# Performance work log

Measured on AMD Instinct MI355X. Metric: run time of the kernel, lower is better.

The kernel has to match this reference:

```python
import jax, jax.numpy as jnp
import numpy as np
import math

B, S, D, H, WD = 8, 2048, 512, 8, 64
DK = D // H


def setup_inputs() -> dict:
    k = jax.random.key(0)
    ks = jax.random.split(k, 16)
    s = 0.02
    return {
        "query": jax.random.normal(ks[0], (B, S, D), jnp.float32),
        "key": jax.random.normal(ks[1], (B, S, D), jnp.float32),
        "value": jax.random.normal(ks[2], (B, S, D), jnp.float32),
        "mask": jax.random.randint(ks[3], (B, S), 0, 2, jnp.int32),
        "segment_weights": jax.random.uniform(ks[4], (B, S, S), jnp.float32),
        # torch Linear weights: [out_features, in_features]
        "Wq": jax.random.normal(ks[5], (D, D), jnp.float32) * s,
        "bq": jnp.zeros((D,), jnp.float32),
        "Wk": jax.random.normal(ks[6], (D, D), jnp.float32) * s,
        "bk": jnp.zeros((D,), jnp.float32),
        "Wv": jax.random.normal(ks[7], (D, D), jnp.float32) * s,
        "bv": jnp.zeros((D,), jnp.float32),
        "Wo": jax.random.normal(ks[8], (D, D), jnp.float32) * s,
        "bo": jnp.zeros((D,), jnp.float32),
        "Wl": jax.random.normal(ks[9], (WD, 1), jnp.float32) * 0.1,
        "bl": jnp.zeros((WD,), jnp.float32),
        "Wr": jax.random.normal(ks[10], (1, WD), jnp.float32) * 0.1,
        "br": jnp.zeros((1,), jnp.float32),
    }


def reference(query, key, value, mask, segment_weights,
              Wq, bq, Wk, bk, Wv, bv, Wo, bo, Wl, bl, Wr, br):
    nb = query.shape[0]
    # segment bias MLP: 1 -> WD -> 1 with leaky_relu(0.2)
    sw = 1.0 / jnp.log(jnp.float32(math.e) + segment_weights)  # [B,S,S]
    hmid = jax.nn.leaky_relu(sw[..., None] * Wl[:, 0] + bl, negative_slope=0.2)  # [B,S,S,WD]
    bias = (hmid @ Wr.T + br)[..., 0]  # [B,S,S]

    def proj(x, W, b):
        return (x @ W.T + b).reshape(nb, -1, H, DK).transpose(0, 2, 1, 3)  # [B,H,S,DK]

    q = proj(query, Wq, bq)
    k = proj(key, Wk, bk)
    v = proj(value, Wv, bv)

    scores = jnp.einsum("bhqd,bhkd->bhqk", q, k) / jnp.float32(math.sqrt(DK))
    scores = scores + bias[:, None]  # broadcast over heads
    # mask [B,S] -> [B,1,S,1]: masks query rows (as in original)
    scores = jnp.where(mask[:, None, :, None] == 0, jnp.float32(-1e9), scores)
    p = jax.nn.softmax(scores, axis=-1)
    x = jnp.einsum("bhqk,bhkd->bhqd", p, v)
    x = x.transpose(0, 2, 1, 3).reshape(nb, -1, H * DK)
    return x @ Wo.T + bo
```

## Files before the change

### kernel.cpp

```cpp
#include <hip/hip_runtime.h>
#include <stdint.h>

#define Bb 8
#define Ss 2048
#define Dd 512
#define Hh 8

typedef unsigned short u16;
typedef __attribute__((ext_vector_type(8))) short s16x8;
typedef __attribute__((ext_vector_type(4))) unsigned short u16x4;
typedef __attribute__((ext_vector_type(4))) float f32x4;
typedef __attribute__((ext_vector_type(2))) float f32x2;

__device__ __forceinline__ u16 f2bf(float f){
  unsigned u = __float_as_uint(f);
  return (u16)((u + 0x7fffu + ((u>>16)&1u)) >> 16);
}

__device__ __forceinline__ unsigned cvtpk_bf16(float lo, float hi){
  unsigned r;
  asm("v_cvt_pk_bf16_f32 %0, %1, %2" : "=v"(r) : "v"(lo), "v"(hi));
  return r;
}

__device__ __forceinline__ void gl_lds16(const void* g, void* l){
  __builtin_amdgcn_global_load_lds((const __attribute__((address_space(1))) unsigned int*)g,
                                   (__attribute__((address_space(3))) unsigned int*)l, 16, 0, 0);
}

#define MFMA32(a,b,c) __builtin_amdgcn_mfma_f32_16x16x32_bf16(a,b,c,0,0,0)

__global__ __launch_bounds__(256) void castw(const float* __restrict__ a, const float* __restrict__ b,
                                             const float* __restrict__ c, const float* __restrict__ d,
                                             u16* __restrict__ o){
  int i = blockIdx.x*256 + threadIdx.x;
  const float* src = (i < 65536) ? a : (i < 131072) ? b : (i < 196608) ? c : d;
  int off = (i & 65535) << 2;
  f32x4 v = *(const f32x4*)(src + off);
  u16x4 r;
  #pragma unroll
  for(int j = 0; j < 4; j++) r[j] = f2bf(v[j]);
  *(u16x4*)(o + ((size_t)(i >> 16) << 18) + off) = r;
}

__global__ void prep(const float* __restrict__ Wl, const float* __restrict__ bl,
                     const float* __restrict__ Wr, const float* __restrict__ br,
                     float* __restrict__ consts){
  int w = threadIdx.x;
  float wl = Wl[w], blv = bl[w], wr = Wr[w];
  float h0 = 0.75f*wl + blv; h0 = h0 > 0.f ? h0 : 0.2f*h0;
  float h1 = 1.00f*wl + blv; h1 = h1 > 0.f ? h1 : 0.2f*h1;
  float f0 = wr*h0, f1 = wr*h1;
  #pragma unroll
  for(int off = 32; off > 0; off >>= 1){
    f0 += __shfl_down(f0, off);
    f1 += __shfl_down(f1, off);
  }
  if(w == 0){
    const float L2E = 1.4426950408889634f;
    float brv = br[0];
    float F0 = f0 + brv, F1 = f1 + brv;
    float C1 = (F1 - F0) * 4.0f;
    float C0 = F0 - 0.75f*C1;
    consts[0] = C1 * L2E * L2E;
    consts[1] = C0 * L2E;
  }
}

template<int MODE>
__global__ __launch_bounds__(256) void gemm_t(const void* __restrict__ Ap, const u16* __restrict__ W,
                                              const float* __restrict__ bias, void* __restrict__ Cp){
  __shared__ __align__(16) u16 As[128*32];
  __shared__ __align__(16) u16 Bs[128*32];
  const int t = threadIdx.x;
  const int lane = t & 63, wv = t >> 6;
  const int quad = lane >> 4, l15 = lane & 15;
  const int m0 = blockIdx.x * 128, n0 = blockIdx.y * 128;
  const int R = (wv >> 1) * 64, Cc = (wv & 1) * 64;
  f32x4 acc[4][4] = {};
  for(int kb = 0; kb < 512; kb += 32){
    __syncthreads();
    #pragma unroll
    for(int i = 0; i < 2; i++){
      int u  = i*256 + t;
      int m  = u >> 2;
      int cc = (u & 3) ^ ((m >> 1) & 3);
      if (MODE == 2){
        gl_lds16((const u16*)Ap + (size_t)(m0 + m)*512 + kb + cc*8, As + (size_t)(i*256 + wv*64)*8);
      } else {
        const float* src = (const float*)Ap + (size_t)(m0 + m)*512 + kb + cc*8;
        f32x4 v0 = *(const f32x4*)src;
        f32x4 v1 = *(const f32x4*)(src + 4);
        s16x8 cv;
        #pragma unroll
        for(int r2 = 0; r2 < 4; r2++){ cv[r2] = (short)f2bf(v0[r2]); cv[4+r2] = (short)f2bf(v1[r2]); }
        *(s16x8*)(As + (size_t)u*8) = cv;
      }
      gl_lds16(W + (size_t)(n0 + m)*512 + kb + cc*8, Bs + (size_t)(i*256 + wv*64)*8);
    }
    __syncthreads();
    s16x8 af[4], bfr[4];
    #pragma unroll
    for(int mi = 0; mi < 4; mi++){
      int m = R + mi*16 + l15;
      int u = (m << 2) | (quad ^ ((m >> 1) & 3));
      af[mi] = *(const s16x8*)(As + (size_t)u*8);
    }
    #pragma unroll
    for(int ni = 0; ni < 4; ni++){
      int n = Cc + ni*16 + l15;
      int u = (n << 2) | (quad ^ ((n >> 1) & 3));
      bfr[ni] = *(const s16x8*)(Bs + (size_t)u*8);
    }
    #pragma unroll
    for(int mi = 0; mi < 4; mi++)
      #pragma unroll
      for(int ni = 0; ni < 4; ni++)
        acc[mi][ni] = MFMA32(af[mi], bfr[ni], acc[mi][ni]);
  }
  #pragma unroll
  for(int ni = 0; ni < 4; ni++){
    int col = n0 + Cc + ni*16 + l15;
    float bv = bias[col];
    #pragma unroll
    for(int mi = 0; mi < 4; mi++){
      int row0 = m0 + R + mi*16 + quad*4;
      #pragma unroll
      for(int r = 0; r < 4; r++){
        float v = acc[mi][ni][r] + bv;
        int row = row0 + r;
        if (MODE == 2)      ((float*)Cp)[(size_t)row*512 + col] = v;
        else if (MODE == 1) ((u16*)Cp)[(size_t)((row >> 11)*512 + col)*2048 + (size_t)(row & 2047)] = f2bf(v);
        else                ((u16*)Cp)[(size_t)row*512 + col] = f2bf(v);
      }
    }
  }
}

__global__ __launch_bounds__(512, 4) void attn(const u16* __restrict__ qp, const u16* __restrict__ kp,
                                               const u16* __restrict__ vt, const float* __restrict__ seg,
                                               const int* __restrict__ mask, const float* __restrict__ consts,
                                               u16* __restrict__ xo){
  __shared__ __align__(16) float bias_s[2][32*36];
  const int t = threadIdx.x;
  const int lane = t & 63, h = t >> 6;
  const int quad = lane >> 4, l15 = lane & 15;
  const int id = (blockIdx.x & 7) * 64 + (blockIdx.x >> 3);
  const int b = id >> 6, q0 = (id & 63) * 32;
  const float C1 = consts[0], C0 = consts[1];
  const int krA = 8*(l15 >> 2) + (l15 & 3);

  s16x8 qf[2][2];
  #pragma unroll
  for(int ni = 0; ni < 2; ni++){
    const u16* qrow = qp + (size_t)(b*Ss + q0 + ni*16 + l15)*Dd + h*64;
    qf[ni][0] = *(const s16x8*)(qrow + quad*8);
    qf[ni][1] = *(const s16x8*)(qrow + 32 + quad*8);
  }
  float mk[2];
  #pragma unroll
  for(int ni = 0; ni < 2; ni++)
    mk[ni] = (mask[b*Ss + q0 + ni*16 + l15] == 0) ? 0.0f : 1.0f;

  f32x4 ot[4][2] = {};
  float lsum[2] = {0.f, 0.f};

  const int sq = t >> 4, sk = (t & 15) * 2;
  const float* segptr = seg + ((size_t)b*Ss + (size_t)(q0 + sq))*Ss + sk;

  const u16* kptr0 = kp + (size_t)(b*Ss + krA    )*Dd + h*64 + quad*8;
  const u16* kptr1 = kp + (size_t)(b*Ss + krA + 4)*Dd + h*64 + quad*8;
  const u16* vptr[4];
  #pragma unroll
  for(int mi2 = 0; mi2 < 4; mi2++)
    vptr[mi2] = vt + (size_t)(b*Dd + h*64 + mi2*16 + l15)*Ss + quad*8;

  f32x2 raw = *(const f32x2*)(segptr);
  f32x2 bvreg;
  #pragma unroll
  for(int j = 0; j < 2; j++)
    bvreg[j] = C1 * __builtin_amdgcn_rcpf(__log2f(2.718281828459045f + raw[j])) + C0;

  for(int k0 = 0; k0 < Ss; k0 += 32){
    float* bs = bias_s[(k0 >> 5) & 1];

    s16x8 kf[2][2];
    kf[0][0] = *(const s16x8*)(kptr0 + (size_t)k0*Dd);
    kf[0][1] = *(const s16x8*)(kptr0 + (size_t)k0*Dd + 32);
    kf[1][0] = *(const s16x8*)(kptr1 + (size_t)k0*Dd);
    kf[1][1] = *(const s16x8*)(kptr1 + (size_t)k0*Dd + 32);
    *(f32x2*)(bs + sq*36 + sk) = bvreg;
    if (k0 + 32 < Ss) raw = *(const f32x2*)(segptr + k0 + 32);

    asm volatile("s_waitcnt lgkmcnt(0)" ::: "memory");
    __builtin_amdgcn_s_barrier();
    __builtin_amdgcn_sched_barrier(0);

    f32x4 st[2][2] = {};
    #pragma unroll
    for(int ks = 0; ks < 2; ks++)
      #pragma unroll
      for(int mi = 0; mi < 2; mi++)
        #pragma unroll
        for(int ni = 0; ni < 2; ni++)
          st[mi][ni] = MFMA32(kf[mi][ks], qf[ni][ks], st[mi][ni]);

    s16x8 vf[4];
    #pragma unroll
    for(int mi2 = 0; mi2 < 4; mi2++)
      vf[mi2] = *(const s16x8*)(vptr[mi2] + k0);

    union { unsigned u[4]; s16x8 v; } P[2];
    #pragma unroll
    for(int mi = 0; mi < 2; mi++)
      #pragma unroll
      for(int ni = 0; ni < 2; ni++){
        f32x4 bb = *(const f32x4*)(bs + (ni*16 + l15)*36 + quad*8 + mi*4);
        f32x4 s = st[mi][ni] * 0.18033688011112042f + bb;
        s *= mk[ni];
        float p[4];
        #pragma unroll
        for(int r = 0; r < 4; r++){
          float sv = __builtin_amdgcn_fmed3f(s[r], -30.f, 30.f);
          p[r] = __builtin_amdgcn_exp2f(sv);
          lsum[ni] += p[r];
        }
        P[ni].u[mi*2 + 0] = cvtpk_bf16(p[0], p[1]);
        P[ni].u[mi*2 + 1] = cvtpk_bf16(p[2], p[3]);
      }

    #pragma unroll
    for(int mi2 = 0; mi2 < 4; mi2++)
      #pragma unroll
      for(int ni = 0; ni < 2; ni++)
        ot[mi2][ni] = MFMA32(vf[mi2], P[ni].v, ot[mi2][ni]);

    if (k0 + 32 < Ss){
      #pragma unroll
      for(int j = 0; j < 2; j++)
        bvreg[j] = C1 * __builtin_amdgcn_rcpf(__log2f(2.718281828459045f + raw[j])) + C0;
    }
  }

  float rl[2];
  #pragma unroll
  for(int ni = 0; ni < 2; ni++){
    float l = lsum[ni];
    l += __shfl_xor(l, 16);
    l += __shfl_xor(l, 32);
    rl[ni] = 1.0f / l;
  }

  #pragma unroll
  for(int ni = 0; ni < 2; ni++)
    #pragma unroll
    for(int mi2 = 0; mi2 < 4; mi2++){
      u16x4 o;
      #pragma unroll
      for(int r = 0; r < 4; r++) o[r] = f2bf(ot[mi2][ni][r] * rl[ni]);
      *(u16x4*)(xo + (size_t)(b*Ss + q0 + ni*16 + l15)*Dd + h*64 + mi2*16 + quad*4) = o;
    }
}

extern "C" void kernel_launch(void* const* d_in, const int* in_sizes, int n_in,
                              void* d_out, int out_size, void* d_ws, size_t ws_size,
                              hipStream_t stream){
  const float* query = (const float*)d_in[0];
  const float* key   = (const float*)d_in[1];
  const float* value = (const float*)d_in[2];
  const int*   mask  = (const int*)d_in[3];
  const float* seg   = (const float*)d_in[4];
  const float* Wq = (const float*)d_in[5];  const float* bq = (const float*)d_in[6];
  const float* Wk = (const float*)d_in[7];  const float* bk = (const float*)d_in[8];
  const float* Wv = (const float*)d_in[9];  const float* bv = (const float*)d_in[10];
  const float* Wo = (const float*)d_in[11]; const float* bo = (const float*)d_in[12];
  const float* Wl = (const float*)d_in[13]; const float* bl = (const float*)d_in[14];
  const float* Wr = (const float*)d_in[15]; const float* br = (const float*)d_in[16];

  char* ws = (char*)d_ws;
  float* consts = (float*)ws;
  u16* Wc  = (u16*)(ws + 4096);
  u16* qp  = (u16*)(ws + ((size_t)4  << 20));
  u16* kp  = (u16*)(ws + ((size_t)20 << 20));
  u16* vt  = (u16*)(ws + ((size_t)36 << 20));
  u16* xo  = qp;
  const size_t WN = (size_t)512*512;

  castw<<<1024, 256, 0, stream>>>(Wq, Wk, Wv, Wo, Wc);
  prep<<<1, 64, 0, stream>>>(Wl, bl, Wr, br, consts);
  gemm_t<0><<<dim3(128,4), 256, 0, stream>>>(query, Wc + 0*WN, bq, qp);
  gemm_t<0><<<dim3(128,4), 256, 0, stream>>>(key,   Wc + 1*WN, bk, kp);
  gemm_t<1><<<dim3(128,4), 256, 0, stream>>>(value, Wc + 2*WN, bv, vt);
  attn<<<512, 512, 0, stream>>>(qp, kp, vt, seg, mask, consts, xo);
  gemm_t<2><<<dim3(128,4), 256, 0, stream>>>(xo, Wc + 3*WN, bo, d_out);
}
```

Before: 573.1 us.

## Stage segment bias in 256-wide chunks to cut per-iteration block barriers

The segment-bias tile in shared memory grows from a double-buffered 32-column tile to a single 256-column tile. Each thread now loads and transforms 16 floats per chunk with vector loads. This means one pair of barriers per 256 keys instead of one barrier per 32 keys, and the inner loop runs without synchronisation, with the V loads hoisted next to the K loads. In exchange, LDS use rises to about 33KB per block, which may limit occupancy, the extra registers may add pressure, and the bias transform is no longer overlapped with the MFMA work.

```diff
diff --git a/kernel.cpp b/kernel.cpp
--- a/kernel.cpp
+++ b/kernel.cpp
@@ -141,7 +141,7 @@
                                                const u16* __restrict__ vt, const float* __restrict__ seg,
                                                const int* __restrict__ mask, const float* __restrict__ consts,
                                                u16* __restrict__ xo){
-  __shared__ __align__(16) float bias_s[2][32*36];
+  __shared__ __align__(16) float bias_s[32*260];
   const int t = threadIdx.x;
   const int lane = t & 63, h = t >> 6;
   const int quad = lane >> 4, l15 = lane & 15;
@@ -165,8 +165,8 @@
   f32x4 ot[4][2] = {};
   float lsum[2] = {0.f, 0.f};
 
-  const int sq = t >> 4, sk = (t & 15) * 2;
-  const float* segptr = seg + ((size_t)b*Ss + (size_t)(q0 + sq))*Ss + sk;
+  const int sq = t >> 4, sc = (t & 15) * 16;
+  const float* segptr = seg + ((size_t)b*Ss + (size_t)(q0 + sq))*Ss + sc;
 
   const u16* kptr0 = kp + (size_t)(b*Ss + krA    )*Dd + h*64 + quad*8;
   const u16* kptr1 = kp + (size_t)(b*Ss + krA + 4)*Dd + h*64 + quad*8;
@@ -175,70 +175,75 @@
   for(int mi2 = 0; mi2 < 4; mi2++)
     vptr[mi2] = vt + (size_t)(b*Dd + h*64 + mi2*16 + l15)*Ss + quad*8;
 
-  f32x2 raw = *(const f32x2*)(segptr);
-  f32x2 bvreg;
-  #pragma unroll
-  for(int j = 0; j < 2; j++)
-    bvreg[j] = C1 * __builtin_amdgcn_rcpf(__log2f(2.718281828459045f + raw[j])) + C0;
-
-  for(int k0 = 0; k0 < Ss; k0 += 32){
-    float* bs = bias_s[(k0 >> 5) & 1];
-
-    s16x8 kf[2][2];
-    kf[0][0] = *(const s16x8*)(kptr0 + (size_t)k0*Dd);
-    kf[0][1] = *(const s16x8*)(kptr0 + (size_t)k0*Dd + 32);
-    kf[1][0] = *(const s16x8*)(kptr1 + (size_t)k0*Dd);
-    kf[1][1] = *(const s16x8*)(kptr1 + (size_t)k0*Dd + 32);
-    *(f32x2*)(bs + sq*36 + sk) = bvreg;
-    if (k0 + 32 < Ss) raw = *(const f32x2*)(segptr + k0 + 32);
-
+  f32x4 sr[4];
+  #pragma unroll
+  for(int j = 0; j < 4; j++) sr[j] = *(const f32x4*)(segptr + j*4);
+
+  for(int K0 = 0; K0 < Ss; K0 += 256){
+    asm volatile("s_waitcnt lgkmcnt(0)" ::: "memory");
+    __builtin_amdgcn_s_barrier();
+    #pragma unroll
+    for(int j = 0; j < 4; j++){
+      f32x4 bv;
+      #pragma unroll
+      for(int r = 0; r < 4; r++)
+        bv[r] = C1 * __builtin_amdgcn_rcpf(__log2f(2.718281828459045f + sr[j][r])) + C0;
+      *(f32x4*)(bias_s + sq*260 + sc + j*4) = bv;
+    }
+    if (K0 + 256 < Ss){
+      #pragma unroll
+      for(int j = 0; j < 4; j++) sr[j] = *(const f32x4*)(segptr + K0 + 256 + j*4);
+    }
     asm volatile("s_waitcnt lgkmcnt(0)" ::: "memory");
     __builtin_amdgcn_s_barrier();
     __builtin_amdgcn_sched_barrier(0);
 
-    f32x4 st[2][2] = {};
-    #pragma unroll
-    for(int ks = 0; ks < 2; ks++)
+    #pragma unroll 2
+    for(int k0 = K0; k0 < K0 + 256; k0 += 32){
+      s16x8 kf[2][2];
+      kf[0][0] = *(const s16x8*)(kptr0 + (size_t)k0*Dd);
+      kf[0][1] = *(const s16x8*)(kptr0 + (size_t)k0*Dd + 32);
+      kf[1][0] = *(const s16x8*)(kptr1 + (size_t)k0*Dd);
+      kf[1][1] = *(const s16x8*)(kptr1 + (size_t)k0*Dd + 32);
+      s16x8 vf[4];
+      #pragma unroll
+      for(int mi2 = 0; mi2 < 4; mi2++)
+        vf[mi2] = *(const s16x8*)(vptr[mi2] + k0);
+
+      f32x4 st[2][2] = {};
+      #pragma unroll
+      for(int ks = 0; ks < 2; ks++)
+        #pragma unroll
+        for(int mi = 0; mi < 2; mi++)
+          #pragma unroll
+          for(int ni = 0; ni < 2; ni++)
+            st[mi][ni] = MFMA32(kf[mi][ks], qf[ni][ks], st[mi][ni]);
+
+      const int koff = k0 - K0;
+      union { unsigned u[4]; s16x8 v; } P[2];
       #pragma unroll
       for(int mi = 0; mi < 2; mi++)
         #pragma unroll
+        for(int ni = 0; ni < 2; ni++){
+          f32x4 bb = *(const f32x4*)(bias_s + (ni*16 + l15)*260 + koff + quad*8 + mi*4);
+          f32x4 s = st[mi][ni] * 0.18033688011112042f + bb;
+          s *= mk[ni];
+          float p[4];
+          #pragma unroll
+          for(int r = 0; r < 4; r++){
+            float sv = __builtin_amdgcn_fmed3f(s[r], -30.f, 30.f);
+            p[r] = __builtin_amdgcn_exp2f(sv);
+            lsum[ni] += p[r];
+          }
+          P[ni].u[mi*2 + 0] = cvtpk_bf16(p[0], p[1]);
+          P[ni].u[mi*2 + 1] = cvtpk_bf16(p[2], p[3]);
+        }
+
+      #pragma unroll
+      for(int mi2 = 0; mi2 < 4; mi2++)
+        #pragma unroll
         for(int ni = 0; ni < 2; ni++)
-          st[mi][ni] = MFMA32(kf[mi][ks], qf[ni][ks], st[mi][ni]);
-
-    s16x8 vf[4];
-    #pragma unroll
-    for(int mi2 = 0; mi2 < 4; mi2++)
-      vf[mi2] = *(const s16x8*)(vptr[mi2] + k0);
-
-    union { unsigned u[4]; s16x8 v; } P[2];
-    #pragma unroll
-    for(int mi = 0; mi < 2; mi++)
-      #pragma unroll
-      for(int ni = 0; ni < 2; ni++){
-        f32x4 bb = *(const f32x4*)(bs + (ni*16 + l15)*36 + quad*8 + mi*4);
-        f32x4 s = st[mi][ni] * 0.18033688011112042f + bb;
-        s *= mk[ni];
-        float p[4];
-        #pragma unroll
-        for(int r = 0; r < 4; r++){
-          float sv = __builtin_amdgcn_fmed3f(s[r], -30.f, 30.f);
-          p[r] = __builtin_amdgcn_exp2f(sv);
-          lsum[ni] += p[r];
-        }
-        P[ni].u[mi*2 + 0] = cvtpk_bf16(p[0], p[1]);
-        P[ni].u[mi*2 + 1] = cvtpk_bf16(p[2], p[3]);
-      }
-
-    #pragma unroll
-    for(int mi2 = 0; mi2 < 4; mi2++)
-      #pragma unroll
-      for(int ni = 0; ni < 2; ni++)
-        ot[mi2][ni] = MFMA32(vf[mi2], P[ni].v, ot[mi2][ni]);
-
-    if (k0 + 32 < Ss){
-      #pragma unroll
-      for(int j = 0; j < 2; j++)
-        bvreg[j] = C1 * __builtin_amdgcn_rcpf(__log2f(2.718281828459045f + raw[j])) + C0;
+          ot[mi2][ni] = MFMA32(vf[mi2], P[ni].v, ot[mi2][ni]);
     }
   }
 
```

After: 640.2 us. 11.7% more time.

## Store K and V projections in MFMA fragment-major layout for contiguous attention loads

Applied to the files above, without the earlier changes.

The K and V projection GEMMs now write their bf16 outputs directly in a per-(batch, key-block, head, fragment, lane) layout that matches the register fragments the attention kernel consumes. Each wave's K and V loads become fully contiguous 16-byte-per-lane reads instead of strided row gathers. This reduces scattered global memory traffic in the attention inner loop. In exchange, the K epilogue does scattered 2-byte stores and the V epilogue writes 8-byte chunks, which makes the projection GEMMs more expensive.

```diff
diff --git a/kernel.cpp b/kernel.cpp
--- a/kernel.cpp
+++ b/kernel.cpp
@@ -122,23 +122,42 @@
   for(int ni = 0; ni < 4; ni++){
     int col = n0 + Cc + ni*16 + l15;
     float bv = bias[col];
+    int hh = col >> 6;
+    int mi2 = (col >> 4) & 3, al15v = col & 15;
+    int w6 = col & 63, ks = w6 >> 5, aqk = (w6 >> 3) & 3, jk = w6 & 7;
     #pragma unroll
     for(int mi = 0; mi < 4; mi++){
       int row0 = m0 + R + mi*16 + quad*4;
-      #pragma unroll
-      for(int r = 0; r < 4; r++){
-        float v = acc[mi][ni][r] + bv;
-        int row = row0 + r;
-        if (MODE == 2)      ((float*)Cp)[(size_t)row*512 + col] = v;
-        else if (MODE == 1) ((u16*)Cp)[(size_t)((row >> 11)*512 + col)*2048 + (size_t)(row & 2047)] = f2bf(v);
-        else                ((u16*)Cp)[(size_t)row*512 + col] = f2bf(v);
+      if (MODE == 1){
+        int bb2 = row0 >> 11, tok = row0 & 2047, kb2 = tok >> 5, kl = tok & 31;
+        int aq = kl >> 3, jb = kl & 7;
+        u16x4 o;
+        #pragma unroll
+        for(int r = 0; r < 4; r++) o[r] = f2bf(acc[mi][ni][r] + bv);
+        size_t off = (((((size_t)bb2*64 + kb2)*8 + hh)*4 + mi2)*64 + (size_t)(aq*16 + al15v))*8 + jb;
+        *(u16x4*)((u16*)Cp + off) = o;
+      } else {
+        #pragma unroll
+        for(int r = 0; r < 4; r++){
+          float v = acc[mi][ni][r] + bv;
+          int row = row0 + r;
+          if (MODE == 2)      ((float*)Cp)[(size_t)row*512 + col] = v;
+          else if (MODE == 3){
+            int bb2 = row >> 11, tok = row & 2047, kb2 = tok >> 5, kl = tok & 31;
+            int kmi = (kl >> 2) & 1;
+            int al15 = 4*(kl >> 3) + (kl & 3);
+            size_t off = (((((size_t)bb2*64 + kb2)*8 + hh)*4 + (ks*2 + kmi))*64 + (size_t)(aqk*16 + al15))*8 + jk;
+            ((u16*)Cp)[off] = f2bf(v);
+          }
+          else                ((u16*)Cp)[(size_t)row*512 + col] = f2bf(v);
+        }
       }
     }
   }
 }
 
-__global__ __launch_bounds__(512, 4) void attn(const u16* __restrict__ qp, const u16* __restrict__ kp,
-                                               const u16* __restrict__ vt, const float* __restrict__ seg,
+__global__ __launch_bounds__(512, 4) void attn(const u16* __restrict__ qp, const u16* __restrict__ kf_g,
+                                               const u16* __restrict__ vf_g, const float* __restrict__ seg,
                                                const int* __restrict__ mask, const float* __restrict__ consts,
                                                u16* __restrict__ xo){
   __shared__ __align__(16) float bias_s[2][32*36];
@@ -148,7 +167,6 @@
   const int id = (blockIdx.x & 7) * 64 + (blockIdx.x >> 3);
   const int b = id >> 6, q0 = (id & 63) * 32;
   const float C1 = consts[0], C0 = consts[1];
-  const int krA = 8*(l15 >> 2) + (l15 & 3);
 
   s16x8 qf[2][2];
   #pragma unroll
@@ -168,12 +186,8 @@
   const int sq = t >> 4, sk = (t & 15) * 2;
   const float* segptr = seg + ((size_t)b*Ss + (size_t)(q0 + sq))*Ss + sk;
 
-  const u16* kptr0 = kp + (size_t)(b*Ss + krA    )*Dd + h*64 + quad*8;
-  const u16* kptr1 = kp + (size_t)(b*Ss + krA + 4)*Dd + h*64 + quad*8;
-  const u16* vptr[4];
-  #pragma unroll
-  for(int mi2 = 0; mi2 < 4; mi2++)
-    vptr[mi2] = vt + (size_t)(b*Dd + h*64 + mi2*16 + l15)*Ss + quad*8;
+  const u16* kfp = kf_g + (size_t)b*1048576 + h*2048 + (size_t)lane*8;
+  const u16* vfp = vf_g + (size_t)b*1048576 + h*2048 + (size_t)lane*8;
 
   f32x2 raw = *(const f32x2*)(segptr);
   f32x2 bvreg;
@@ -184,11 +198,12 @@
   for(int k0 = 0; k0 < Ss; k0 += 32){
     float* bs = bias_s[(k0 >> 5) & 1];
 
+    const u16* kfb = kfp + (size_t)k0*512;
     s16x8 kf[2][2];
-    kf[0][0] = *(const s16x8*)(kptr0 + (size_t)k0*Dd);
-    kf[0][1] = *(const s16x8*)(kptr0 + (size_t)k0*Dd + 32);
-    kf[1][0] = *(const s16x8*)(kptr1 + (size_t)k0*Dd);
-    kf[1][1] = *(const s16x8*)(kptr1 + (size_t)k0*Dd + 32);
+    kf[0][0] = *(const s16x8*)(kfb);
+    kf[1][0] = *(const s16x8*)(kfb + 512);
+    kf[0][1] = *(const s16x8*)(kfb + 1024);
+    kf[1][1] = *(const s16x8*)(kfb + 1536);
     *(f32x2*)(bs + sq*36 + sk) = bvreg;
     if (k0 + 32 < Ss) raw = *(const f32x2*)(segptr + k0 + 32);
 
@@ -205,10 +220,11 @@
         for(int ni = 0; ni < 2; ni++)
           st[mi][ni] = MFMA32(kf[mi][ks], qf[ni][ks], st[mi][ni]);
 
+    const u16* vfb = vfp + (size_t)k0*512;
     s16x8 vf[4];
     #pragma unroll
     for(int mi2 = 0; mi2 < 4; mi2++)
-      vf[mi2] = *(const s16x8*)(vptr[mi2] + k0);
+      vf[mi2] = *(const s16x8*)(vfb + mi2*512);
 
     union { unsigned u[4]; s16x8 v; } P[2];
     #pragma unroll
@@ -281,16 +297,16 @@
   float* consts = (float*)ws;
   u16* Wc  = (u16*)(ws + 4096);
   u16* qp  = (u16*)(ws + ((size_t)4  << 20));
-  u16* kp  = (u16*)(ws + ((size_t)20 << 20));
-  u16* vt  = (u16*)(ws + ((size_t)36 << 20));
+  u16* kfb = (u16*)(ws + ((size_t)20 << 20));
+  u16* vfb = (u16*)(ws + ((size_t)36 << 20));
   u16* xo  = qp;
   const size_t WN = (size_t)512*512;
 
   castw<<<1024, 256, 0, stream>>>(Wq, Wk, Wv, Wo, Wc);
   prep<<<1, 64, 0, stream>>>(Wl, bl, Wr, br, consts);
   gemm_t<0><<<dim3(128,4), 256, 0, stream>>>(query, Wc + 0*WN, bq, qp);
-  gemm_t<0><<<dim3(128,4), 256, 0, stream>>>(key,   Wc + 1*WN, bk, kp);
-  gemm_t<1><<<dim3(128,4), 256, 0, stream>>>(value, Wc + 2*WN, bv, vt);
-  attn<<<512, 512, 0, stream>>>(qp, kp, vt, seg, mask, consts, xo);
+  gemm_t<3><<<dim3(128,4), 256, 0, stream>>>(key,   Wc + 1*WN, bk, kfb);
+  gemm_t<1><<<dim3(128,4), 256, 0, stream>>>(value, Wc + 2*WN, bv, vfb);
+  attn<<<512, 512, 0, stream>>>(qp, kfb, vfb, seg, mask, consts, xo);
   gemm_t<2><<<dim3(128,4), 256, 0, stream>>>(xo, Wc + 3*WN, bo, d_out);
 }
```

New measurement: 478.7 us. -16.5%, faster.
